# Kernel tuning notes

Hardware: AMD Instinct MI355X
Metric: run time of the kernel (lower is better)

Reference implementation:

```python
import jax, jax.numpy as jnp
import numpy as np

DIM = 1024
INTER = 512
E = 16            # n_routed_experts
TOPK = 4          # n_activated_experts
N_GROUPS = 4
TOPK_GROUPS = 2
ROUTE_SCALE = 1.0
INIT_STD = 0.02
B, S = 2, 1024


def setup_inputs() -> dict:
    key = jax.random.key(0)
    ks = jax.random.split(key, 8)
    return {
        "x": jax.random.normal(ks[0], (B, S, DIM), jnp.float32),
        "gate_w": jax.random.normal(ks[1], (E, DIM), jnp.float32) * INIT_STD,
        "gate_bias": jnp.zeros((E,), jnp.float32),
        "w1": jax.random.normal(ks[2], (E, INTER, DIM), jnp.float32) * INIT_STD,
        "w2": jax.random.normal(ks[3], (E, DIM, INTER), jnp.float32) * INIT_STD,
        "w3": jax.random.normal(ks[4], (E, INTER, DIM), jnp.float32) * INIT_STD,
        "ws1": jax.random.normal(ks[5], (INTER, DIM), jnp.float32) * INIT_STD,
        "ws2": jax.random.normal(ks[6], (DIM, INTER), jnp.float32) * INIT_STD,
        "ws3": jax.random.normal(ks[7], (INTER, DIM), jnp.float32) * INIT_STD,
    }


def reference(x, gate_w, gate_bias, w1, w2, w3, ws1, ws2, ws3):
    Bx, Sx, D = x.shape
    T = Bx * Sx
    xf = x.reshape(T, D)

    # ---- Gate: sigmoid scores + expert bias, group-limited top-k ----
    scores = jax.nn.sigmoid(xf @ gate_w.T)          # [T, E]
    original_scores = scores
    s = scores + gate_bias                          # bias only affects selection
    sg = s.reshape(T, N_GROUPS, E // N_GROUPS)
    group_scores = sg.max(axis=-1)                  # [T, G]
    _, gidx = jax.lax.top_k(group_scores, TOPK_GROUPS)
    keep = jnp.zeros((T, N_GROUPS), bool).at[jnp.arange(T)[:, None], gidx].set(True)
    s_masked = jnp.where(keep[:, :, None], sg, -jnp.inf).reshape(T, E)
    _, idx = jax.lax.top_k(s_masked, TOPK)          # [T, topk]
    weights = jnp.take_along_axis(original_scores, idx, axis=1) * ROUTE_SCALE

    # combine weights as sparse [T, E] matrix (scatter of top-k weights)
    comb = jnp.zeros((T, E), x.dtype).at[jnp.arange(T)[:, None], idx].add(weights)

    # ---- Routed experts: SwiGLU per expert, weighted combine ----
    h1 = jnp.einsum('td,eid->tei', xf, w1)          # [T, E, inter]
    h3 = jnp.einsum('td,eid->tei', xf, w3)
    h = jax.nn.silu(h1) * h3
    y = jnp.einsum('tei,edi,te->td', h, w2, comb)   # weighted combine

    # ---- Shared expert (SwiGLU MLP) ----
    z = (jax.nn.silu(xf @ ws1.T) * (xf @ ws3.T)) @ ws2.T

    return (y + z).reshape(Bx, Sx, D)
```

## Files before the change

kernel.cpp:

```cpp
#include <hip/hip_runtime.h>

#define T_TOK  2048
#define DIMD   1024
#define INTERI 512
#define NEXP   16
#define NSEG   17

typedef __bf16 bf16x8 __attribute__((ext_vector_type(8)));
typedef float  f32x4  __attribute__((ext_vector_type(4)));
typedef float  f32x8  __attribute__((ext_vector_type(8)));
typedef unsigned short u16x8 __attribute__((ext_vector_type(8)));

#define SW(row, c) ((((c) + ((row) >> 1)) & 3) * 8)

__device__ __forceinline__ unsigned short f2b(float f) {
    union { float f; unsigned int u; } c; c.f = f;
    unsigned int u = c.u;
    unsigned int r = (u + 0x7FFFu + ((u >> 16) & 1u)) >> 16;
    return (unsigned short)r;
}

__device__ __forceinline__ bf16x8 cvt8(f32x8 v) {
    bf16x8 r;
#pragma unroll
    for (int i = 0; i < 8; ++i) r[i] = (__bf16)v[i];
    return r;
}

__device__ __forceinline__ void lds_barrier() {
    asm volatile("s_waitcnt lgkmcnt(0)" ::: "memory");
    __builtin_amdgcn_s_barrier();
}

__global__ __launch_bounds__(256) void cvt_w_kernel(
    const float* __restrict__ w1,  const float* __restrict__ w3,
    const float* __restrict__ ws1, const float* __restrict__ ws3,
    unsigned short* __restrict__ w1b,  unsigned short* __restrict__ w3b,
    unsigned short* __restrict__ ws1b, unsigned short* __restrict__ ws3b)
{
    int g = blockIdx.x * 256 + threadIdx.x;
    const float* s; unsigned short* d; int i;
    if      (g < 1048576) { s = w1;  d = w1b;  i = g; }
    else if (g < 2097152) { s = w3;  d = w3b;  i = g - 1048576; }
    else if (g < 2162688) { s = ws1; d = ws1b; i = g - 2097152; }
    else                  { s = ws3; d = ws3b; i = g - 2162688; }
    float4 v0 = ((const float4*)s)[2 * i];
    float4 v1 = ((const float4*)s)[2 * i + 1];
    u16x8 o;
    o[0] = f2b(v0.x); o[1] = f2b(v0.y); o[2] = f2b(v0.z); o[3] = f2b(v0.w);
    o[4] = f2b(v1.x); o[5] = f2b(v1.y); o[6] = f2b(v1.z); o[7] = f2b(v1.w);
    ((u16x8*)d)[i] = o;
}

__global__ __launch_bounds__(256) void gate_score_kernel(
    const float* __restrict__ x, const float* __restrict__ gw,
    const float* __restrict__ gb,
    unsigned* __restrict__ sel, float4* __restrict__ selw,
    unsigned short* __restrict__ xb)
{
    int tok  = blockIdx.x * 4 + (threadIdx.x >> 6);
    int lane = threadIdx.x & 63;
    const float* xp = x + (size_t)tok * DIMD;
    float xv[16];
#pragma unroll
    for (int j = 0; j < 16; ++j) xv[j] = xp[j * 64 + lane];

    unsigned short* xbp = xb + (size_t)tok * DIMD;
#pragma unroll
    for (int j = 0; j < 16; ++j) xbp[j * 64 + lane] = f2b(xv[j]);

    float sc[16];
#pragma unroll
    for (int e = 0; e < 16; ++e) {
        const float* gwe = gw + e * DIMD;
        float p0 = 0.f, p1 = 0.f;
#pragma unroll
        for (int j = 0; j < 16; j += 2) {
            p0 += xv[j]     * gwe[j * 64 + lane];
            p1 += xv[j + 1] * gwe[(j + 1) * 64 + lane];
        }
        float p = p0 + p1;
#pragma unroll
        for (int o = 32; o; o >>= 1) p += __shfl_xor(p, o, 64);
        sc[e] = p;
    }
    if (lane != 0) return;

    float orig[16], s[16];
#pragma unroll
    for (int e = 0; e < 16; ++e) {
        orig[e] = 1.f / (1.f + expf(-sc[e]));
        s[e] = orig[e] + gb[e];
    }
    float gmax[4];
#pragma unroll
    for (int g = 0; g < 4; ++g) {
        float m = s[4 * g];
        for (int j = 1; j < 4; ++j) m = fmaxf(m, s[4 * g + j]);
        gmax[g] = m;
    }
    int g0 = 0;
    for (int g = 1; g < 4; ++g) if (gmax[g] > gmax[g0]) g0 = g;
    int g1 = -1;
    for (int g = 0; g < 4; ++g) { if (g == g0) continue; if (g1 < 0 || gmax[g] > gmax[g1]) g1 = g; }
    unsigned keep = (0xFu << (4 * g0)) | (0xFu << (4 * g1));
    unsigned used = 0;
    unsigned pk = 0;
    float w4[4];
    for (int j = 0; j < 4; ++j) {
        int best = -1;
        for (int e = 0; e < 16; ++e) {
            if (!((keep >> e) & 1u) || ((used >> e) & 1u)) continue;
            if (best < 0 || s[e] > s[best]) best = e;
        }
        used |= 1u << best;
        pk |= ((unsigned)best) << (4 * j);
        w4[j] = orig[best];
    }
    sel[tok] = pk;
    selw[tok] = make_float4(w4[0], w4[1], w4[2], w4[3]);
}

__global__ __launch_bounds__(256) void build_lists_kernel(
    const unsigned* __restrict__ sel, const float4* __restrict__ selw,
    int* __restrict__ counts, int* __restrict__ lst, float* __restrict__ lstw)
{
    const int e    = blockIdx.x;
    const int tid  = threadIdx.x;
    const int wave = tid >> 6;
    const int lane = tid & 63;

    __shared__ int wsum[4];
    __shared__ int basev;
    if (tid == 0) basev = 0;
    __syncthreads();

    for (int c = 0; c < T_TOK / 256; ++c) {
        int t = c * 256 + tid;
        unsigned s = sel[t];
        int match = -1;
#pragma unroll
        for (int j = 0; j < 4; ++j)
            if (((s >> (4 * j)) & 15u) == (unsigned)e) match = j;
        unsigned long long m = __ballot(match >= 0);
        int wpre = __popcll(m & ((1ull << lane) - 1ull));
        if (lane == 0) wsum[wave] = __popcll(m);
        __syncthreads();
        int pre = basev;
        for (int wv = 0; wv < wave; ++wv) pre += wsum[wv];
        if (match >= 0) {
            int pos = pre + wpre;
            lst [e * T_TOK + pos] = t | (match << 16);
            const float* wp = (const float*)&selw[t];
            lstw[e * T_TOK + pos] = wp[match];
        }
        __syncthreads();
        if (tid == 0) basev += wsum[0] + wsum[1] + wsum[2] + wsum[3];
        __syncthreads();
    }
    if (tid == 0) counts[e] = basev;
}

__global__ __launch_bounds__(256, 2) void gemm1_kernel(
    const unsigned short* __restrict__ xb,
    const unsigned short* __restrict__ w1b,
    const unsigned short* __restrict__ w3b,
    const unsigned short* __restrict__ ws1b,
    const unsigned short* __restrict__ ws3b,
    const int* __restrict__ counts,
    const int* __restrict__ lst,
    unsigned short* __restrict__ H)
{
    int b = blockIdx.x;
    int seg, mt, nt;
    if (b < 1024) {
        int xcd = b & 7, slot = b >> 3;
        seg = xcd + 8 * (slot >> 6);
        int tile = slot & 63;
        mt = tile >> 2; nt = tile & 3;
    } else {
        seg = NEXP;
        int tile = b - 1024;
        mt = tile >> 2; nt = tile & 3;
    }
    const int n_e = (seg == NEXP) ? T_TOK : counts[seg];
    const int m0  = mt * 128;
    if (m0 >= n_e) return;
    const int n0  = nt * 128;

    const unsigned short* w1p = (seg == NEXP) ? ws1b : w1b + (size_t)seg * INTERI * DIMD;
    const unsigned short* w3p = (seg == NEXP) ? ws3b : w3b + (size_t)seg * INTERI * DIMD;
    const int* lste = lst + seg * T_TOK;

    __shared__ __align__(16) unsigned short lA [2][128][32];
    __shared__ __align__(16) unsigned short lB1[2][128][32];
    __shared__ __align__(16) unsigned short lB3[2][128][32];

    const int tid  = threadIdx.x;
    const int wave = tid >> 6;
    const int lane = tid & 63;
    const int quad = lane >> 4;
    const int lrow = lane & 15;
    const int r4   = tid >> 2;
    const int ct   = tid & 3;

    int ra0 = m0 + r4;       if (ra0 > n_e - 1) ra0 = n_e - 1;
    int ra1 = m0 + r4 + 64;  if (ra1 > n_e - 1) ra1 = n_e - 1;
    int tok0 = (seg == NEXP) ? ra0 : (lste[ra0] & 0xFFFF);
    int tok1 = (seg == NEXP) ? ra1 : (lste[ra1] & 0xFFFF);
    const unsigned short* gA0  = xb  + (size_t)tok0 * DIMD + ct * 8;
    const unsigned short* gA1  = xb  + (size_t)tok1 * DIMD + ct * 8;
    const unsigned short* gB1a = w1p + (size_t)(n0 + r4)      * DIMD + ct * 8;
    const unsigned short* gB1b = w1p + (size_t)(n0 + r4 + 64) * DIMD + ct * 8;
    const unsigned short* gB3a = w3p + (size_t)(n0 + r4)      * DIMD + ct * 8;
    const unsigned short* gB3b = w3p + (size_t)(n0 + r4 + 64) * DIMD + ct * 8;

    bf16x8 pa[2][2], pb1[2][2], pb3[2][2];

#define G1LOAD(k0) do { _Pragma("unroll") for (int kk = 0; kk < 2; ++kk) { \
    pa [0][kk] = *(const bf16x8*)(gA0  + (k0) + kk * 32); \
    pa [1][kk] = *(const bf16x8*)(gA1  + (k0) + kk * 32); \
    pb1[0][kk] = *(const bf16x8*)(gB1a + (k0) + kk * 32); \
    pb1[1][kk] = *(const bf16x8*)(gB1b + (k0) + kk * 32); \
    pb3[0][kk] = *(const bf16x8*)(gB3a + (k0) + kk * 32); \
    pb3[1][kk] = *(const bf16x8*)(gB3b + (k0) + kk * 32); } } while (0)

#define G1STORE() do { _Pragma("unroll") for (int kk = 0; kk < 2; ++kk) { \
    *(bf16x8*)&lA [kk][r4]     [SW(r4, ct)]      = pa [0][kk]; \
    *(bf16x8*)&lA [kk][64 + r4][SW(64 + r4, ct)] = pa [1][kk]; \
    *(bf16x8*)&lB1[kk][r4]     [SW(r4, ct)]      = pb1[0][kk]; \
    *(bf16x8*)&lB1[kk][64 + r4][SW(64 + r4, ct)] = pb1[1][kk]; \
    *(bf16x8*)&lB3[kk][r4]     [SW(r4, ct)]      = pb3[0][kk]; \
    *(bf16x8*)&lB3[kk][64 + r4][SW(64 + r4, ct)] = pb3[1][kk]; } } while (0)

    f32x4 acc1[4][4], acc3[4][4];
    const f32x4 zero = {0.f, 0.f, 0.f, 0.f};
#pragma unroll
    for (int i = 0; i < 4; ++i)
#pragma unroll
        for (int j = 0; j < 4; ++j) { acc1[i][j] = zero; acc3[i][j] = zero; }

    const int wm = (wave & 1) * 64;
    const int wn = (wave >> 1) * 64;

    G1LOAD(0);
    const int NK = DIMD / 64;
    for (int it = 0; it < NK; ++it) {
        G1STORE();
        lds_barrier();
        if (it + 1 < NK) G1LOAD((it + 1) * 64);
#pragma unroll
        for (int kk = 0; kk < 2; ++kk) {
            bf16x8 a[4], b1[4], b3[4];
#pragma unroll
            for (int t = 0; t < 4; ++t) {
                int rr = wm + t * 16 + lrow;
                a[t] = *(const bf16x8*)&lA[kk][rr][SW(rr, quad)];
            }
#pragma unroll
            for (int t = 0; t < 4; ++t) {
                int rc = wn + t * 16 + lrow;
                b1[t] = *(const bf16x8*)&lB1[kk][rc][SW(rc, quad)];
                b3[t] = *(const bf16x8*)&lB3[kk][rc][SW(rc, quad)];
            }
#pragma unroll
            for (int i = 0; i < 4; ++i)
#pragma unroll
                for (int j = 0; j < 4; ++j) {
                    acc1[i][j] = __builtin_amdgcn_mfma_f32_16x16x32_bf16(a[i], b1[j], acc1[i][j], 0, 0, 0);
                    acc3[i][j] = __builtin_amdgcn_mfma_f32_16x16x32_bf16(a[i], b3[j], acc3[i][j], 0, 0, 0);
                }
        }
        lds_barrier();
    }
#undef G1LOAD
#undef G1STORE

    unsigned short* Hseg = H + (size_t)seg * T_TOK * INTERI;
#pragma unroll
    for (int i = 0; i < 4; ++i) {
        int rbase = m0 + wm + i * 16 + quad * 4;
#pragma unroll
        for (int r = 0; r < 4; ++r) {
            int row = rbase + r;
            if (row >= n_e) continue;
            unsigned short* hrow = Hseg + (size_t)row * INTERI + n0 + wn + lrow;
#pragma unroll
            for (int j = 0; j < 4; ++j) {
                float v1 = acc1[i][j][r];
                float v3 = acc3[i][j][r];
                float hv = (v1 / (1.f + __expf(-v1))) * v3;
                hrow[j * 16] = f2b(hv);
            }
        }
    }
}

__global__ __launch_bounds__(256, 2) void gemm2_kernel(
    const unsigned short* __restrict__ H,
    const float* __restrict__ w2f,
    const float* __restrict__ ws2f,
    const int* __restrict__ counts,
    const int* __restrict__ lst,
    const float* __restrict__ lstw,
    float* __restrict__ P)
{
    int b = blockIdx.x;
    int seg, mt, nt;
    if (b < 2048) {
        int xcd = b & 7, slot = b >> 3;
        seg = xcd + 8 * (slot >> 7);
        int tile = slot & 127;
        mt = tile >> 3; nt = tile & 7;
    } else {
        seg = NEXP;
        int tile = b - 2048;
        mt = tile >> 3; nt = tile & 7;
    }
    const int n_e = (seg == NEXP) ? T_TOK : counts[seg];
    const int m0  = mt * 128;
    if (m0 >= n_e) return;
    const int n0  = nt * 128;

    const float* w2p = (seg == NEXP) ? ws2f : w2f + (size_t)seg * DIMD * INTERI;
    const unsigned short* Hseg = H + (size_t)seg * T_TOK * INTERI;

    __shared__ __align__(16) unsigned short lA[2][128][32];
    __shared__ __align__(16) unsigned short lB[2][128][32];

    const int tid  = threadIdx.x;
    const int wave = tid >> 6;
    const int lane = tid & 63;
    const int quad = lane >> 4;
    const int lrow = lane & 15;
    const int r4   = tid >> 2;
    const int ct   = tid & 3;

    int ra0 = m0 + r4;       if (ra0 > n_e - 1) ra0 = n_e - 1;
    int ra1 = m0 + r4 + 64;  if (ra1 > n_e - 1) ra1 = n_e - 1;
    const unsigned short* gA0 = Hseg + (size_t)ra0 * INTERI + ct * 8;
    const unsigned short* gA1 = Hseg + (size_t)ra1 * INTERI + ct * 8;
    const float* gB0 = w2p + (size_t)(n0 + r4)      * INTERI + ct * 8;
    const float* gB1 = w2p + (size_t)(n0 + r4 + 64) * INTERI + ct * 8;

    bf16x8 pa[2][2];
    f32x8  pb[2][2];

#define G2LOAD(k0) do { _Pragma("unroll") for (int kk = 0; kk < 2; ++kk) { \
    pa[0][kk] = *(const bf16x8*)(gA0 + (k0) + kk * 32); \
    pa[1][kk] = *(const bf16x8*)(gA1 + (k0) + kk * 32); \
    pb[0][kk] = *(const f32x8*)(gB0 + (k0) + kk * 32); \
    pb[1][kk] = *(const f32x8*)(gB1 + (k0) + kk * 32); } } while (0)

#define G2STORE() do { _Pragma("unroll") for (int kk = 0; kk < 2; ++kk) { \
    *(bf16x8*)&lA[kk][r4]     [SW(r4, ct)]      = pa[0][kk]; \
    *(bf16x8*)&lA[kk][64 + r4][SW(64 + r4, ct)] = pa[1][kk]; \
    *(bf16x8*)&lB[kk][r4]     [SW(r4, ct)]      = cvt8(pb[0][kk]); \
    *(bf16x8*)&lB[kk][64 + r4][SW(64 + r4, ct)] = cvt8(pb[1][kk]); } } while (0)

    f32x4 acc[4][4];
    const f32x4 zero = {0.f, 0.f, 0.f, 0.f};
#pragma unroll
    for (int i = 0; i < 4; ++i)
#pragma unroll
        for (int j = 0; j < 4; ++j) acc[i][j] = zero;

    const int wm = (wave & 1) * 64;
    const int wn = (wave >> 1) * 64;

    G2LOAD(0);
    const int NK = INTERI / 64;
    for (int it = 0; it < NK; ++it) {
        G2STORE();
        lds_barrier();
        if (it + 1 < NK) G2LOAD((it + 1) * 64);
#pragma unroll
        for (int kk = 0; kk < 2; ++kk) {
            bf16x8 a[4], bv[4];
#pragma unroll
            for (int t = 0; t < 4; ++t) {
                int rr = wm + t * 16 + lrow;
                a[t] = *(const bf16x8*)&lA[kk][rr][SW(rr, quad)];
            }
#pragma unroll
            for (int t = 0; t < 4; ++t) {
                int rc = wn + t * 16 + lrow;
                bv[t] = *(const bf16x8*)&lB[kk][rc][SW(rc, quad)];
            }
#pragma unroll
            for (int i = 0; i < 4; ++i)
#pragma unroll
                for (int j = 0; j < 4; ++j)
                    acc[i][j] = __builtin_amdgcn_mfma_f32_16x16x32_bf16(a[i], bv[j], acc[i][j], 0, 0, 0);
        }
        lds_barrier();
    }
#undef G2LOAD
#undef G2STORE

#pragma unroll
    for (int i = 0; i < 4; ++i) {
        int rbase = m0 + wm + i * 16 + quad * 4;
#pragma unroll
        for (int r = 0; r < 4; ++r) {
            int row = rbase + r;
            if (row >= n_e) continue;
            int tok, slot; float wt;
            if (seg == NEXP) { tok = row; slot = 4; wt = 1.f; }
            else {
                int ent = lst[seg * T_TOK + row];
                tok = ent & 0xFFFF; slot = ent >> 16;
                wt = lstw[seg * T_TOK + row];
            }
            float* prow = P + ((size_t)slot * T_TOK + tok) * DIMD + n0 + wn + lrow;
#pragma unroll
            for (int j = 0; j < 4; ++j)
                prow[j * 16] = wt * acc[i][j][r];
        }
    }
}

__global__ __launch_bounds__(256) void combine_kernel(
    const float4* __restrict__ P, float4* __restrict__ y)
{
    const int i = blockIdx.x * 256 + threadIdx.x;
    const size_t plane = (size_t)T_TOK * DIMD / 4;
    float4 a = P[i];
    float4 b = P[plane + i];
    float4 c = P[2 * plane + i];
    float4 d = P[3 * plane + i];
    float4 e = P[4 * plane + i];
    float4 o;
    o.x = a.x + b.x + c.x + d.x + e.x;
    o.y = a.y + b.y + c.y + d.y + e.y;
    o.z = a.z + b.z + c.z + d.z + e.z;
    o.w = a.w + b.w + c.w + d.w + e.w;
    y[i] = o;
}

extern "C" void kernel_launch(void* const* d_in, const int* in_sizes, int n_in,
                              void* d_out, int out_size, void* d_ws, size_t ws_size,
                              hipStream_t stream)
{
    const float* x   = (const float*)d_in[0];
    const float* gw  = (const float*)d_in[1];
    const float* gb  = (const float*)d_in[2];
    const float* w1  = (const float*)d_in[3];
    const float* w2  = (const float*)d_in[4];
    const float* w3  = (const float*)d_in[5];
    const float* ws1 = (const float*)d_in[6];
    const float* ws2 = (const float*)d_in[7];
    const float* ws3 = (const float*)d_in[8];

    char* base = (char*)d_ws;
    size_t off = 0;
    auto alloc = [&](size_t bytes) {
        char* q = base + off; off += (bytes + 255) & ~(size_t)255; return q;
    };
    unsigned short* xb   = (unsigned short*)alloc((size_t)T_TOK * DIMD * 2);
    unsigned short* w1b  = (unsigned short*)alloc((size_t)NEXP * INTERI * DIMD * 2);
    unsigned short* w3b  = (unsigned short*)alloc((size_t)NEXP * INTERI * DIMD * 2);
    unsigned short* ws1b = (unsigned short*)alloc((size_t)INTERI * DIMD * 2);
    unsigned short* ws3b = (unsigned short*)alloc((size_t)INTERI * DIMD * 2);
    unsigned short* Hb   = (unsigned short*)alloc((size_t)NSEG * T_TOK * INTERI * 2);
    int*            cnts = (int*)alloc(NEXP * 4);
    int*            lstp = (int*)alloc((size_t)NEXP * T_TOK * 4);
    float*          lstw = (float*)alloc((size_t)NEXP * T_TOK * 4);
    unsigned*       selp = (unsigned*)alloc((size_t)T_TOK * 4);
    float4*         selw = (float4*)alloc((size_t)T_TOK * 16);
    float*          Pb   = (float*)alloc((size_t)5 * T_TOK * DIMD * 4);

    cvt_w_kernel<<<8704, 256, 0, stream>>>(w1, w3, ws1, ws3, w1b, w3b, ws1b, ws3b);
    gate_score_kernel<<<T_TOK / 4, 256, 0, stream>>>(x, gw, gb, selp, selw, xb);
    build_lists_kernel<<<NEXP, 256, 0, stream>>>(selp, selw, cnts, lstp, lstw);
    gemm1_kernel<<<1088, 256, 0, stream>>>(xb, w1b, w3b, ws1b, ws3b, cnts, lstp, Hb);
    gemm2_kernel<<<2176, 256, 0, stream>>>(Hb, w2, ws2, cnts, lstp, lstw, Pb);
    combine_kernel<<<(T_TOK * DIMD / 4) / 256, 256, 0, stream>>>((const float4*)Pb, (float4*)d_out);
}
```

Before: 247.5 us.

## Merge prep kernels, build expert lists with atomics, double-buffer GEMM prefetch

Measured after the change: 336.0 us. +35.8%, slower.

```diff
diff --git a/kernel.cpp b/kernel.cpp
--- a/kernel.cpp
+++ b/kernel.cpp
@@ -9,7 +9,6 @@
 typedef __bf16 bf16x8 __attribute__((ext_vector_type(8)));
 typedef float  f32x4  __attribute__((ext_vector_type(4)));
 typedef float  f32x8  __attribute__((ext_vector_type(8)));
-typedef unsigned short u16x8 __attribute__((ext_vector_type(8)));
 
 #define SW(row, c) ((((c) + ((row) >> 1)) & 3) * 8)
 
@@ -32,33 +31,29 @@
     __builtin_amdgcn_s_barrier();
 }
 
-__global__ __launch_bounds__(256) void cvt_w_kernel(
+__global__ __launch_bounds__(256) void prep_kernel(
     const float* __restrict__ w1,  const float* __restrict__ w3,
     const float* __restrict__ ws1, const float* __restrict__ ws3,
-    unsigned short* __restrict__ w1b,  unsigned short* __restrict__ w3b,
-    unsigned short* __restrict__ ws1b, unsigned short* __restrict__ ws3b)
-{
-    int g = blockIdx.x * 256 + threadIdx.x;
-    const float* s; unsigned short* d; int i;
-    if      (g < 1048576) { s = w1;  d = w1b;  i = g; }
-    else if (g < 2097152) { s = w3;  d = w3b;  i = g - 1048576; }
-    else if (g < 2162688) { s = ws1; d = ws1b; i = g - 2097152; }
-    else                  { s = ws3; d = ws3b; i = g - 2162688; }
-    float4 v0 = ((const float4*)s)[2 * i];
-    float4 v1 = ((const float4*)s)[2 * i + 1];
-    u16x8 o;
-    o[0] = f2b(v0.x); o[1] = f2b(v0.y); o[2] = f2b(v0.z); o[3] = f2b(v0.w);
-    o[4] = f2b(v1.x); o[5] = f2b(v1.y); o[6] = f2b(v1.z); o[7] = f2b(v1.w);
-    ((u16x8*)d)[i] = o;
-}
-
-__global__ __launch_bounds__(256) void gate_score_kernel(
+    bf16x8* __restrict__ w1b,  bf16x8* __restrict__ w3b,
+    bf16x8* __restrict__ ws1b, bf16x8* __restrict__ ws3b,
     const float* __restrict__ x, const float* __restrict__ gw,
     const float* __restrict__ gb,
-    unsigned* __restrict__ sel, float4* __restrict__ selw,
+    int* __restrict__ cnts, int* __restrict__ lstp, float* __restrict__ lstw,
     unsigned short* __restrict__ xb)
 {
-    int tok  = blockIdx.x * 4 + (threadIdx.x >> 6);
+    const int b = blockIdx.x;
+    if (b < 8704) {
+        int g = b * 256 + threadIdx.x;
+        const float* s; bf16x8* d; int i;
+        if      (g < 1048576) { s = w1;  d = w1b;  i = g; }
+        else if (g < 2097152) { s = w3;  d = w3b;  i = g - 1048576; }
+        else if (g < 2162688) { s = ws1; d = ws1b; i = g - 2097152; }
+        else                  { s = ws3; d = ws3b; i = g - 2162688; }
+        f32x8 v = ((const f32x8*)s)[i];
+        d[i] = cvt8(v);
+        return;
+    }
+    int tok  = (b - 8704) * 4 + (threadIdx.x >> 6);
     int lane = threadIdx.x & 63;
     const float* xp = x + (size_t)tok * DIMD;
     float xv[16];
@@ -105,8 +100,6 @@
     for (int g = 0; g < 4; ++g) { if (g == g0) continue; if (g1 < 0 || gmax[g] > gmax[g1]) g1 = g; }
     unsigned keep = (0xFu << (4 * g0)) | (0xFu << (4 * g1));
     unsigned used = 0;
-    unsigned pk = 0;
-    float w4[4];
     for (int j = 0; j < 4; ++j) {
         int best = -1;
         for (int e = 0; e < 16; ++e) {
@@ -114,51 +107,10 @@
             if (best < 0 || s[e] > s[best]) best = e;
         }
         used |= 1u << best;
-        pk |= ((unsigned)best) << (4 * j);
-        w4[j] = orig[best];
-    }
-    sel[tok] = pk;
-    selw[tok] = make_float4(w4[0], w4[1], w4[2], w4[3]);
-}
-
-__global__ __launch_bounds__(256) void build_lists_kernel(
-    const unsigned* __restrict__ sel, const float4* __restrict__ selw,
-    int* __restrict__ counts, int* __restrict__ lst, float* __restrict__ lstw)
-{
-    const int e    = blockIdx.x;
-    const int tid  = threadIdx.x;
-    const int wave = tid >> 6;
-    const int lane = tid & 63;
-
-    __shared__ int wsum[4];
-    __shared__ int basev;
-    if (tid == 0) basev = 0;
-    __syncthreads();
-
-    for (int c = 0; c < T_TOK / 256; ++c) {
-        int t = c * 256 + tid;
-        unsigned s = sel[t];
-        int match = -1;
-#pragma unroll
-        for (int j = 0; j < 4; ++j)
-            if (((s >> (4 * j)) & 15u) == (unsigned)e) match = j;
-        unsigned long long m = __ballot(match >= 0);
-        int wpre = __popcll(m & ((1ull << lane) - 1ull));
-        if (lane == 0) wsum[wave] = __popcll(m);
-        __syncthreads();
-        int pre = basev;
-        for (int wv = 0; wv < wave; ++wv) pre += wsum[wv];
-        if (match >= 0) {
-            int pos = pre + wpre;
-            lst [e * T_TOK + pos] = t | (match << 16);
-            const float* wp = (const float*)&selw[t];
-            lstw[e * T_TOK + pos] = wp[match];
-        }
-        __syncthreads();
-        if (tid == 0) basev += wsum[0] + wsum[1] + wsum[2] + wsum[3];
-        __syncthreads();
-    }
-    if (tid == 0) counts[e] = basev;
+        int pos = atomicAdd(&cnts[best], 1);
+        lstp[best * T_TOK + pos] = tok | (j << 16);
+        lstw[best * T_TOK + pos] = orig[best];
+    }
 }
 
 __global__ __launch_bounds__(256, 2) void gemm1_kernel(
@@ -215,23 +167,33 @@
     const unsigned short* gB3a = w3p + (size_t)(n0 + r4)      * DIMD + ct * 8;
     const unsigned short* gB3b = w3p + (size_t)(n0 + r4 + 64) * DIMD + ct * 8;
 
-    bf16x8 pa[2][2], pb1[2][2], pb3[2][2];
-
-#define G1LOAD(k0) do { _Pragma("unroll") for (int kk = 0; kk < 2; ++kk) { \
-    pa [0][kk] = *(const bf16x8*)(gA0  + (k0) + kk * 32); \
-    pa [1][kk] = *(const bf16x8*)(gA1  + (k0) + kk * 32); \
-    pb1[0][kk] = *(const bf16x8*)(gB1a + (k0) + kk * 32); \
-    pb1[1][kk] = *(const bf16x8*)(gB1b + (k0) + kk * 32); \
-    pb3[0][kk] = *(const bf16x8*)(gB3a + (k0) + kk * 32); \
-    pb3[1][kk] = *(const bf16x8*)(gB3b + (k0) + kk * 32); } } while (0)
-
-#define G1STORE() do { _Pragma("unroll") for (int kk = 0; kk < 2; ++kk) { \
-    *(bf16x8*)&lA [kk][r4]     [SW(r4, ct)]      = pa [0][kk]; \
-    *(bf16x8*)&lA [kk][64 + r4][SW(64 + r4, ct)] = pa [1][kk]; \
-    *(bf16x8*)&lB1[kk][r4]     [SW(r4, ct)]      = pb1[0][kk]; \
-    *(bf16x8*)&lB1[kk][64 + r4][SW(64 + r4, ct)] = pb1[1][kk]; \
-    *(bf16x8*)&lB3[kk][r4]     [SW(r4, ct)]      = pb3[0][kk]; \
-    *(bf16x8*)&lB3[kk][64 + r4][SW(64 + r4, ct)] = pb3[1][kk]; } } while (0)
+    bf16x8 pa[2][2];
+    bf16x8 p1A[2][2], p1B[2][2];
+    bf16x8 p3A[2][2], p3B[2][2];
+
+#define G1LOADA(k0) do { _Pragma("unroll") for (int kk = 0; kk < 2; ++kk) { \
+    pa[0][kk] = *(const bf16x8*)(gA0 + (k0) + kk * 32); \
+    pa[1][kk] = *(const bf16x8*)(gA1 + (k0) + kk * 32); } } while (0)
+
+#define G1LOADW_A(k0) do { _Pragma("unroll") for (int kk = 0; kk < 2; ++kk) { \
+    p1A[0][kk] = *(const bf16x8*)(gB1a + (k0) + kk * 32); \
+    p1A[1][kk] = *(const bf16x8*)(gB1b + (k0) + kk * 32); \
+    p3A[0][kk] = *(const bf16x8*)(gB3a + (k0) + kk * 32); \
+    p3A[1][kk] = *(const bf16x8*)(gB3b + (k0) + kk * 32); } } while (0)
+
+#define G1LOADW_B(k0) do { _Pragma("unroll") for (int kk = 0; kk < 2; ++kk) { \
+    p1B[0][kk] = *(const bf16x8*)(gB1a + (k0) + kk * 32); \
+    p1B[1][kk] = *(const bf16x8*)(gB1b + (k0) + kk * 32); \
+    p3B[0][kk] = *(const bf16x8*)(gB3a + (k0) + kk * 32); \
+    p3B[1][kk] = *(const bf16x8*)(gB3b + (k0) + kk * 32); } } while (0)
+
+#define G1STORE(P1, P3) do { _Pragma("unroll") for (int kk = 0; kk < 2; ++kk) { \
+    *(bf16x8*)&lA [kk][r4]     [SW(r4, ct)]      = pa[0][kk]; \
+    *(bf16x8*)&lA [kk][64 + r4][SW(64 + r4, ct)] = pa[1][kk]; \
+    *(bf16x8*)&lB1[kk][r4]     [SW(r4, ct)]      = P1[0][kk]; \
+    *(bf16x8*)&lB1[kk][64 + r4][SW(64 + r4, ct)] = P1[1][kk]; \
+    *(bf16x8*)&lB3[kk][r4]     [SW(r4, ct)]      = P3[0][kk]; \
+    *(bf16x8*)&lB3[kk][64 + r4][SW(64 + r4, ct)] = P3[1][kk]; } } while (0)
 
     f32x4 acc1[4][4], acc3[4][4];
     const f32x4 zero = {0.f, 0.f, 0.f, 0.f};
@@ -243,38 +205,44 @@
     const int wm = (wave & 1) * 64;
     const int wn = (wave >> 1) * 64;
 
-    G1LOAD(0);
-    const int NK = DIMD / 64;
-    for (int it = 0; it < NK; ++it) {
-        G1STORE();
-        lds_barrier();
-        if (it + 1 < NK) G1LOAD((it + 1) * 64);
-#pragma unroll
-        for (int kk = 0; kk < 2; ++kk) {
-            bf16x8 a[4], b1[4], b3[4];
-#pragma unroll
-            for (int t = 0; t < 4; ++t) {
-                int rr = wm + t * 16 + lrow;
-                a[t] = *(const bf16x8*)&lA[kk][rr][SW(rr, quad)];
-            }
-#pragma unroll
-            for (int t = 0; t < 4; ++t) {
-                int rc = wn + t * 16 + lrow;
-                b1[t] = *(const bf16x8*)&lB1[kk][rc][SW(rc, quad)];
-                b3[t] = *(const bf16x8*)&lB3[kk][rc][SW(rc, quad)];
-            }
-#pragma unroll
-            for (int i = 0; i < 4; ++i)
-#pragma unroll
-                for (int j = 0; j < 4; ++j) {
-                    acc1[i][j] = __builtin_amdgcn_mfma_f32_16x16x32_bf16(a[i], b1[j], acc1[i][j], 0, 0, 0);
-                    acc3[i][j] = __builtin_amdgcn_mfma_f32_16x16x32_bf16(a[i], b3[j], acc3[i][j], 0, 0, 0);
-                }
-        }
-        lds_barrier();
-    }
-#undef G1LOAD
+#define G1COMPUTE() do { _Pragma("unroll") for (int kk = 0; kk < 2; ++kk) { \
+    bf16x8 a[4], bv[4]; \
+    _Pragma("unroll") for (int t = 0; t < 4; ++t) { \
+        int rr = wm + t * 16 + lrow; \
+        a[t] = *(const bf16x8*)&lA[kk][rr][SW(rr, quad)]; } \
+    _Pragma("unroll") for (int t = 0; t < 4; ++t) { \
+        int rc = wn + t * 16 + lrow; \
+        bv[t] = *(const bf16x8*)&lB1[kk][rc][SW(rc, quad)]; } \
+    _Pragma("unroll") for (int i = 0; i < 4; ++i) \
+    _Pragma("unroll") for (int j = 0; j < 4; ++j) \
+        acc1[i][j] = __builtin_amdgcn_mfma_f32_16x16x32_bf16(a[i], bv[j], acc1[i][j], 0, 0, 0); \
+    _Pragma("unroll") for (int t = 0; t < 4; ++t) { \
+        int rc = wn + t * 16 + lrow; \
+        bv[t] = *(const bf16x8*)&lB3[kk][rc][SW(rc, quad)]; } \
+    _Pragma("unroll") for (int i = 0; i < 4; ++i) \
+    _Pragma("unroll") for (int j = 0; j < 4; ++j) \
+        acc3[i][j] = __builtin_amdgcn_mfma_f32_16x16x32_bf16(a[i], bv[j], acc3[i][j], 0, 0, 0); \
+    } } while (0)
+
+    G1LOADA(0); G1LOADW_A(0); G1LOADW_B(64);
+    for (int it2 = 0; it2 < 8; ++it2) {
+        G1STORE(p1A, p3A);
+        lds_barrier();
+        G1LOADA((2 * it2 + 1) * 64);
+        if (it2 < 7) G1LOADW_A((2 * it2 + 2) * 64);
+        G1COMPUTE();
+        lds_barrier();
+        G1STORE(p1B, p3B);
+        lds_barrier();
+        if (it2 < 7) { G1LOADA((2 * it2 + 2) * 64); G1LOADW_B((2 * it2 + 3) * 64); }
+        G1COMPUTE();
+        lds_barrier();
+    }
+#undef G1LOADA
+#undef G1LOADW_A
+#undef G1LOADW_B
 #undef G1STORE
+#undef G1COMPUTE
 
     unsigned short* Hseg = H + (size_t)seg * T_TOK * INTERI;
 #pragma unroll
@@ -343,20 +311,26 @@
     const float* gB0 = w2p + (size_t)(n0 + r4)      * INTERI + ct * 8;
     const float* gB1 = w2p + (size_t)(n0 + r4 + 64) * INTERI + ct * 8;
 
-    bf16x8 pa[2][2];
-    f32x8  pb[2][2];
-
-#define G2LOAD(k0) do { _Pragma("unroll") for (int kk = 0; kk < 2; ++kk) { \
-    pa[0][kk] = *(const bf16x8*)(gA0 + (k0) + kk * 32); \
-    pa[1][kk] = *(const bf16x8*)(gA1 + (k0) + kk * 32); \
-    pb[0][kk] = *(const f32x8*)(gB0 + (k0) + kk * 32); \
-    pb[1][kk] = *(const f32x8*)(gB1 + (k0) + kk * 32); } } while (0)
-
-#define G2STORE() do { _Pragma("unroll") for (int kk = 0; kk < 2; ++kk) { \
-    *(bf16x8*)&lA[kk][r4]     [SW(r4, ct)]      = pa[0][kk]; \
-    *(bf16x8*)&lA[kk][64 + r4][SW(64 + r4, ct)] = pa[1][kk]; \
-    *(bf16x8*)&lB[kk][r4]     [SW(r4, ct)]      = cvt8(pb[0][kk]); \
-    *(bf16x8*)&lB[kk][64 + r4][SW(64 + r4, ct)] = cvt8(pb[1][kk]); } } while (0)
+    bf16x8 paA[2][2], paB[2][2];
+    f32x8  pbA[2][2], pbB[2][2];
+
+#define G2LOAD_A(k0) do { _Pragma("unroll") for (int kk = 0; kk < 2; ++kk) { \
+    paA[0][kk] = *(const bf16x8*)(gA0 + (k0) + kk * 32); \
+    paA[1][kk] = *(const bf16x8*)(gA1 + (k0) + kk * 32); \
+    pbA[0][kk] = *(const f32x8*)(gB0 + (k0) + kk * 32); \
+    pbA[1][kk] = *(const f32x8*)(gB1 + (k0) + kk * 32); } } while (0)
+
+#define G2LOAD_B(k0) do { _Pragma("unroll") for (int kk = 0; kk < 2; ++kk) { \
+    paB[0][kk] = *(const bf16x8*)(gA0 + (k0) + kk * 32); \
+    paB[1][kk] = *(const bf16x8*)(gA1 + (k0) + kk * 32); \
+    pbB[0][kk] = *(const f32x8*)(gB0 + (k0) + kk * 32); \
+    pbB[1][kk] = *(const f32x8*)(gB1 + (k0) + kk * 32); } } while (0)
+
+#define G2STORE(PA, PB) do { _Pragma("unroll") for (int kk = 0; kk < 2; ++kk) { \
+    *(bf16x8*)&lA[kk][r4]     [SW(r4, ct)]      = PA[0][kk]; \
+    *(bf16x8*)&lA[kk][64 + r4][SW(64 + r4, ct)] = PA[1][kk]; \
+    *(bf16x8*)&lB[kk][r4]     [SW(r4, ct)]      = cvt8(PB[0][kk]); \
+    *(bf16x8*)&lB[kk][64 + r4][SW(64 + r4, ct)] = cvt8(PB[1][kk]); } } while (0)
 
     f32x4 acc[4][4];
     const f32x4 zero = {0.f, 0.f, 0.f, 0.f};
@@ -368,35 +342,36 @@
     const int wm = (wave & 1) * 64;
     const int wn = (wave >> 1) * 64;
 
-    G2LOAD(0);
-    const int NK = INTERI / 64;
-    for (int it = 0; it < NK; ++it) {
-        G2STORE();
-        lds_barrier();
-        if (it + 1 < NK) G2LOAD((it + 1) * 64);
-#pragma unroll
-        for (int kk = 0; kk < 2; ++kk) {
-            bf16x8 a[4], bv[4];
-#pragma unroll
-            for (int t = 0; t < 4; ++t) {
-                int rr = wm + t * 16 + lrow;
-                a[t] = *(const bf16x8*)&lA[kk][rr][SW(rr, quad)];
-            }
-#pragma unroll
-            for (int t = 0; t < 4; ++t) {
-                int rc = wn + t * 16 + lrow;
-                bv[t] = *(const bf16x8*)&lB[kk][rc][SW(rc, quad)];
-            }
-#pragma unroll
-            for (int i = 0; i < 4; ++i)
-#pragma unroll
-                for (int j = 0; j < 4; ++j)
-                    acc[i][j] = __builtin_amdgcn_mfma_f32_16x16x32_bf16(a[i], bv[j], acc[i][j], 0, 0, 0);
-        }
-        lds_barrier();
-    }
-#undef G2LOAD
+#define G2COMPUTE() do { _Pragma("unroll") for (int kk = 0; kk < 2; ++kk) { \
+    bf16x8 a[4], bv[4]; \
+    _Pragma("unroll") for (int t = 0; t < 4; ++t) { \
+        int rr = wm + t * 16 + lrow; \
+        a[t] = *(const bf16x8*)&lA[kk][rr][SW(rr, quad)]; } \
+    _Pragma("unroll") for (int t = 0; t < 4; ++t) { \
+        int rc = wn + t * 16 + lrow; \
+        bv[t] = *(const bf16x8*)&lB[kk][rc][SW(rc, quad)]; } \
+    _Pragma("unroll") for (int i = 0; i < 4; ++i) \
+    _Pragma("unroll") for (int j = 0; j < 4; ++j) \
+        acc[i][j] = __builtin_amdgcn_mfma_f32_16x16x32_bf16(a[i], bv[j], acc[i][j], 0, 0, 0); \
+    } } while (0)
+
+    G2LOAD_A(0); G2LOAD_B(64);
+    for (int it2 = 0; it2 < 4; ++it2) {
+        G2STORE(paA, pbA);
+        lds_barrier();
+        if (it2 < 3) G2LOAD_A((2 * it2 + 2) * 64);
+        G2COMPUTE();
+        lds_barrier();
+        G2STORE(paB, pbB);
+        lds_barrier();
+        if (it2 < 3) G2LOAD_B((2 * it2 + 3) * 64);
+        G2COMPUTE();
+        lds_barrier();
+    }
+#undef G2LOAD_A
+#undef G2LOAD_B
 #undef G2STORE
+#undef G2COMPUTE
 
 #pragma unroll
     for (int i = 0; i < 4; ++i) {
@@ -466,13 +441,13 @@
     int*            cnts = (int*)alloc(NEXP * 4);
     int*            lstp = (int*)alloc((size_t)NEXP * T_TOK * 4);
     float*          lstw = (float*)alloc((size_t)NEXP * T_TOK * 4);
-    unsigned*       selp = (unsigned*)alloc((size_t)T_TOK * 4);
-    float4*         selw = (float4*)alloc((size_t)T_TOK * 16);
     float*          Pb   = (float*)alloc((size_t)5 * T_TOK * DIMD * 4);
 
-    cvt_w_kernel<<<8704, 256, 0, stream>>>(w1, w3, ws1, ws3, w1b, w3b, ws1b, ws3b);
-    gate_score_kernel<<<T_TOK / 4, 256, 0, stream>>>(x, gw, gb, selp, selw, xb);
-    build_lists_kernel<<<NEXP, 256, 0, stream>>>(selp, selw, cnts, lstp, lstw);
+    hipMemsetAsync(cnts, 0, NEXP * sizeof(int), stream);
+    prep_kernel<<<9216, 256, 0, stream>>>(w1, w3, ws1, ws3,
+                                          (bf16x8*)w1b, (bf16x8*)w3b,
+                                          (bf16x8*)ws1b, (bf16x8*)ws3b,
+                                          x, gw, gb, cnts, lstp, lstw, xb);
     gemm1_kernel<<<1088, 256, 0, stream>>>(xb, w1b, w3b, ws1b, ws3b, cnts, lstp, Hb);
     gemm2_kernel<<<2176, 256, 0, stream>>>(Hb, w2, ws2, cnts, lstp, lstw, Pb);
     combine_kernel<<<(T_TOK * DIMD / 4) / 256, 256, 0, stream>>>((const float4*)Pb, (float4*)d_out);
```
